# Kernel tuning notes

Measured on AMD Instinct MI355X. Metric: run time of the kernel, lower is better.

## Reference

```python
import jax, jax.numpy as jnp
import numpy as np
from jax import lax

SEQ_LEN, PRED_LEN, C_IN, D_MODEL, KS = 96, 48, 7, 128, 5
PAD = (KS - 1) // 2


def setup_inputs() -> dict:
    key = jax.random.key(0)
    ks = jax.random.split(key, 20)
    B = 512
    s = 0.02
    inp = {
        "x_enc": jax.random.normal(ks[0], (B, SEQ_LEN, C_IN), jnp.float32),
        "x_mark": jax.random.randint(ks[1], (B, SEQ_LEN, 4), 0, 7),
        "y_mark": jax.random.randint(ks[2], (B, SEQ_LEN + PRED_LEN, 4), 0, 7),
        # temporal embedding tables
        "hour_emb": jax.random.normal(ks[3], (24, D_MODEL)) * s,
        "weekday_emb": jax.random.normal(ks[4], (7, D_MODEL)) * s,
        "day_emb": jax.random.normal(ks[5], (32, D_MODEL)) * s,
        "month_emb": jax.random.normal(ks[6], (13, D_MODEL)) * s,
        # value embedding Linear(C_IN -> D_MODEL)
        "W_val": jax.random.normal(ks[7], (D_MODEL, C_IN)) * s,
        "b_val": jnp.zeros((D_MODEL,)),
        # three Conv1d(D_MODEL, D_MODEL, KS)
        "conv1_w": jax.random.normal(ks[8], (D_MODEL, D_MODEL, KS)) * s,
        "conv1_b": jnp.zeros((D_MODEL,)),
        "conv2_w": jax.random.normal(ks[9], (D_MODEL, D_MODEL, KS)) * s,
        "conv2_b": jnp.zeros((D_MODEL,)),
        "conv3_w": jax.random.normal(ks[10], (D_MODEL, D_MODEL, KS)) * s,
        "conv3_b": jnp.zeros((D_MODEL,)),
        # GRU (PyTorch layout: 3*D rows ordered [r, z, n])
        "gru_Wi": jax.random.normal(ks[11], (3 * D_MODEL, D_MODEL)) * s,
        "gru_Wh": jax.random.normal(ks[12], (3 * D_MODEL, D_MODEL)) * s,
        "gru_bi": jnp.zeros((3 * D_MODEL,)),
        "gru_bh": jnp.zeros((3 * D_MODEL,)),
        # fc Linear(D_MODEL -> C_IN)
        "fc_w": jax.random.normal(ks[13], (C_IN, D_MODEL)) * s,
        "fc_b": jnp.zeros((C_IN,)),
    }
    return inp


def _conv1d(x, w, b):
    # x: [B, D, T], w: [O, I, K]
    y = lax.conv_general_dilated(x, w, window_strides=(1,), padding=[(PAD, PAD)],
                                 dimension_numbers=("NCH", "OIH", "NCH"))
    return y + b[None, :, None]


def _gru_last(x, Wi, Wh, bi, bh):
    # x: [B, T, D] -> final hidden state [B, D] (PyTorch GRU equations)
    B, T, D = x.shape
    gx = jnp.einsum("btd,gd->btg", x, Wi) + bi  # [B, T, 3D]
    h0 = jnp.zeros((B, D), x.dtype)

    def step(h, gxt):
        gh = h @ Wh.T + bh
        r = jax.nn.sigmoid(gxt[:, :D] + gh[:, :D])
        z = jax.nn.sigmoid(gxt[:, D:2 * D] + gh[:, D:2 * D])
        n = jnp.tanh(gxt[:, 2 * D:] + r * gh[:, 2 * D:])
        return (1.0 - z) * n + z * h, None

    h_last, _ = lax.scan(step, h0, jnp.swapaxes(gx, 0, 1))
    return h_last


def reference(x_enc, x_mark, y_mark,
              hour_emb, weekday_emb, day_emb, month_emb,
              W_val, b_val,
              conv1_w, conv1_b, conv2_w, conv2_b, conv3_w, conv3_b,
              gru_Wi, gru_Wh, gru_bi, gru_bh, fc_w, fc_b):
    B = x_enc.shape[0]
    # temporal embedding for the full y_mark window (pointwise; precompute once)
    temb = (hour_emb[y_mark[:, :, 0]] + weekday_emb[y_mark[:, :, 1]]
            + day_emb[y_mark[:, :, 2]] + month_emb[y_mark[:, :, 3]])  # [B, L, D]

    x_cat = jnp.concatenate([x_enc, jnp.zeros((B, PRED_LEN, C_IN), x_enc.dtype)], axis=1)

    def one_step(x_cat, i):
        xw = lax.dynamic_slice(x_cat, (0, i, 0), (B, SEQ_LEN, C_IN))
        tw = lax.dynamic_slice(temb, (0, i, 0), (B, SEQ_LEN, D_MODEL))
        x = jnp.einsum("btc,dc->btd", xw, W_val) + b_val + tw  # [B, T, D]
        x = jnp.swapaxes(x, 1, 2)  # [B, D, T]
        x = jax.nn.relu(_conv1d(x, conv1_w, conv1_b))
        x = jax.nn.relu(_conv1d(x, conv2_w, conv2_b))
        x = jax.nn.relu(_conv1d(x, conv3_w, conv3_b))
        x = jnp.swapaxes(x, 1, 2)  # [B, T, D]
        h = _gru_last(x, gru_Wi, gru_Wh, gru_bi, gru_bh)  # [B, D]
        pred = h @ fc_w.T + fc_b  # [B, C]
        x_cat = lax.dynamic_update_slice(x_cat, pred[:, None, :], (0, SEQ_LEN + i, 0))
        return x_cat, None

    x_cat, _ = lax.scan(one_step, x_cat, jnp.arange(PRED_LEN))
    return x_cat[:, -PRED_LEN:, :]
```

## Files before the change

kernel.cpp:

```cpp
#include <hip/hip_runtime.h>

#define B_SZ 512
#define SEQ 96
#define PRED 48
#define TOT 144
#define CIN 7
#define DM 128
#define GDIM 384
#define KS 5

#define CSTR 132
#define ASUB (20*CSTR)
#define WROW 136
#define SWZ(o) ((o) + ((((o) >> 6)) << 2))

#define W_CONV (KS*DM*DM)
#define OFF_WIT (3*W_CONV)
#define OFF_WHT (3*W_CONV + DM*GDIM)
#define W_TOTAL (3*W_CONV + 2*DM*GDIM)

__device__ float g_gxg[(size_t)B_SZ*TOT*GDIM];
__device__ float g_gxe[B_SZ*12*GDIM];
__device__ float g_wT[W_TOTAL];

__global__ void prep_weights(const float* __restrict__ w1, const float* __restrict__ w2,
                             const float* __restrict__ w3, const float* __restrict__ Wi,
                             const float* __restrict__ Wh) {
    int tid = blockIdx.x*256 + threadIdx.x;
    if (tid < 3*W_CONV) {
        int l = tid / W_CONV, r = tid % W_CONV;
        int o = r & 127, c = (r >> 7) & 127, k = r >> 14;
        const float* w = (l==0) ? w1 : ((l==1) ? w2 : w3);
        g_wT[tid] = w[o*(DM*KS) + c*KS + k];
    } else if (tid < W_TOTAL) {
        int r = tid - 3*W_CONV;
        int m = r / (DM*GDIM), q = r % (DM*GDIM);
        int g = q % GDIM, c = q / GDIM;
        const float* W = (m==0) ? Wi : Wh;
        g_wT[tid] = W[g*DM + c];
    }
}

template<int NJ>
__device__ __forceinline__ void fma8(float (&acc)[NJ][8], int j, float a,
                                     const float4& wA, const float4& wB) {
    acc[j][0] = fmaf(a, wA.x, acc[j][0]);
    acc[j][1] = fmaf(a, wA.y, acc[j][1]);
    acc[j][2] = fmaf(a, wA.z, acc[j][2]);
    acc[j][3] = fmaf(a, wA.w, acc[j][3]);
    acc[j][4] = fmaf(a, wB.x, acc[j][4]);
    acc[j][5] = fmaf(a, wB.y, acc[j][5]);
    acc[j][6] = fmaf(a, wB.z, acc[j][6]);
    acc[j][7] = fmaf(a, wB.w, acc[j][7]);
}

__device__ __forceinline__ void stage_conv_chunk(float* __restrict__ wbuf,
                                                 const float* __restrict__ wT,
                                                 int cc, int tid) {
    const int cj = tid >> 5, oo = (tid & 31) * 4;
    #pragma unroll
    for (int k = 0; k < KS; ++k)
        *(float4*)(wbuf + (k*8 + cj)*WROW + SWZ(oo)) =
            *(const float4*)(wT + (k*DM + cc*8 + cj)*DM + oo);
}

__device__ __forceinline__ void stage_conv_chunk512(float* __restrict__ wbuf,
                                                    const float* __restrict__ wT,
                                                    int cc, int tid) {
    const int cj = tid >> 6, oo = (tid & 63) * 2;
    #pragma unroll
    for (int k = 0; k < KS; ++k)
        *(float2*)(wbuf + (k*8 + cj)*WROW + SWZ(oo)) =
            *(const float2*)(wT + (k*DM + cc*8 + cj)*DM + oo);
}

template<int NJ>
__device__ __forceinline__ void conv_layer_chunked(float* __restrict__ buf,
                                                   float* __restrict__ wbuf,
                                                   const float* __restrict__ wT,
                                                   const float* __restrict__ bias,
                                                   int nrow, int winO, int tid) {
    const int og = tid & 15, ttg = tid >> 4;
    const int o0 = og*8, so0 = SWZ(o0), r0 = ttg*NJ;
    const bool act = (r0 < nrow);
    float acc[NJ][8];
    #pragma unroll
    for (int u = 0; u < 8; ++u) {
        float bv = bias[o0+u];
        #pragma unroll
        for (int j = 0; j < NJ; ++j) acc[j][u] = bv;
    }
    for (int cc = 0; cc < DM/8; ++cc) {
        __syncthreads();
        stage_conv_chunk(wbuf, wT, cc, tid);
        __syncthreads();
        if (act) {
            const int c0 = cc*8;
            #pragma unroll
            for (int cj = 0; cj < 8; cj += 2) {
                float2 a2[NJ+4];
                #pragma unroll
                for (int m = 0; m < NJ+4; ++m)
                    a2[m] = *(const float2*)(buf + (r0+m)*CSTR + c0 + cj);
                #pragma unroll
                for (int k = 0; k < KS; ++k) {
                    const float4 wA0 = *(const float4*)(wbuf + (k*8+cj)*WROW + so0);
                    const float4 wB0 = *(const float4*)(wbuf + (k*8+cj)*WROW + so0 + 4);
                    const float4 wA1 = *(const float4*)(wbuf + (k*8+cj+1)*WROW + so0);
                    const float4 wB1 = *(const float4*)(wbuf + (k*8+cj+1)*WROW + so0 + 4);
                    #pragma unroll
                    for (int j = 0; j < NJ; ++j) {
                        fma8(acc, j, a2[j+k].x, wA0, wB0);
                        fma8(acc, j, a2[j+k].y, wA1, wB1);
                    }
                }
            }
        }
    }
    __syncthreads();
    if (act) {
        #pragma unroll
        for (int j = 0; j < NJ; ++j) {
            int q = r0 + j, w = winO + q;
            bool valid = (w >= 0) && (w < SEQ);
            #pragma unroll
            for (int u = 0; u < 8; ++u)
                buf[q*CSTR + o0+u] = valid ? fmaxf(acc[j][u], 0.f) : 0.f;
        }
    }
    __syncthreads();
}

__launch_bounds__(256, 3)
__global__ void init_kernel(const float* __restrict__ x_enc,
                            const int* __restrict__ y_mark,
                            const float* __restrict__ hour_e, const float* __restrict__ wk_e,
                            const float* __restrict__ day_e, const float* __restrict__ mon_e,
                            const float* __restrict__ W_val, const float* __restrict__ b_val,
                            const float* __restrict__ b1, const float* __restrict__ b2,
                            const float* __restrict__ b3, const float* __restrict__ gbi) {
    __shared__ float buf[60*CSTR];
    __shared__ float wbuf[KS*8*WROW];
    const int tid = threadIdx.x;
    const int b = blockIdx.x;
    const int cs = blockIdx.y * 48;

    for (int e = tid; e < 60*DM; e += 256) {
        int q = e >> 7, d = e & 127;
        int w = cs - 6 + q;
        float v = 0.f;
        if (w >= 0 && w < SEQ) {
            const float* xr = x_enc + (b*SEQ + w)*CIN;
            v = b_val[d];
            #pragma unroll
            for (int c = 0; c < CIN; ++c) v = fmaf(xr[c], W_val[d*CIN + c], v);
            const int* ym = y_mark + (b*TOT + w)*4;
            v += hour_e[ym[0]*DM + d] + wk_e[ym[1]*DM + d]
               + day_e[ym[2]*DM + d] + mon_e[ym[3]*DM + d];
        }
        buf[q*CSTR + d] = v;
    }
    conv_layer_chunked<4>(buf, wbuf, g_wT,            b1, 56, cs - 4, tid);
    conv_layer_chunked<4>(buf, wbuf, g_wT + W_CONV,   b2, 52, cs - 2, tid);
    conv_layer_chunked<3>(buf, wbuf, g_wT + 2*W_CONV, b3, 48, cs,     tid);

    const int og = tid & 15, ttg = tid >> 4;
    const int g0 = og*24, r0 = ttg*3;
    const float* WiT = g_wT + OFF_WIT;
    float ga[3][24];
    #pragma unroll
    for (int e = 0; e < 24; ++e) {
        float bv = gbi[g0+e];
        #pragma unroll
        for (int j = 0; j < 3; ++j) ga[j][e] = bv;
    }
    for (int cc = 0; cc < DM/8; ++cc) {
        __syncthreads();
        #pragma unroll
        for (int s = 0; s < 3; ++s)
            ((float4*)wbuf)[s*256 + tid] = ((const float4*)(WiT + cc*8*GDIM))[s*256 + tid];
        __syncthreads();
        const int c0 = cc*8;
        #pragma unroll
        for (int cj = 0; cj < 8; cj += 2) {
            float2 a2[3];
            #pragma unroll
            for (int m = 0; m < 3; ++m)
                a2[m] = *(const float2*)(buf + (r0+m)*CSTR + c0 + cj);
            float4 w4[6];
            #pragma unroll
            for (int q = 0; q < 6; ++q)
                w4[q] = *(const float4*)(wbuf + cj*GDIM + g0 + q*4);
            const float* wv = (const float*)w4;
            #pragma unroll
            for (int j = 0; j < 3; ++j)
                #pragma unroll
                for (int e = 0; e < 24; ++e)
                    ga[j][e] = fmaf(a2[j].x, wv[e], ga[j][e]);
            #pragma unroll
            for (int q = 0; q < 6; ++q)
                w4[q] = *(const float4*)(wbuf + (cj+1)*GDIM + g0 + q*4);
            #pragma unroll
            for (int j = 0; j < 3; ++j)
                #pragma unroll
                for (int e = 0; e < 24; ++e)
                    ga[j][e] = fmaf(a2[j].y, wv[e], ga[j][e]);
        }
    }
    #pragma unroll
    for (int j = 0; j < 3; ++j) {
        int w = cs + r0 + j;
        if (w >= 6 && w < 90) {
            float* gxo = g_gxg + ((size_t)b*TOT + w)*GDIM + g0;
            #pragma unroll
            for (int q = 0; q < 6; ++q)
                *(float4*)(gxo + q*4) = *(const float4*)&ga[j][q*4];
        }
    }
}

__device__ __forceinline__ void mlayer512(float* __restrict__ abuf, float* __restrict__ wbuf,
                                          const float* __restrict__ wT,
                                          const float* __restrict__ bias,
                                          int R, int off, int tid) {
    const int og = tid & 15, ttg = tid >> 4;
    const int o0 = og*8, so0 = SWZ(o0);
    const bool act = (ttg < 2*R);
    int s = 0, r0 = 0;
    if (act) { s = ttg / R; r0 = ttg - s*R; }
    float* in = abuf + s*ASUB;
    float acc[1][8];
    #pragma unroll
    for (int u = 0; u < 8; ++u) acc[0][u] = bias[o0+u];
    for (int cc = 0; cc < DM/8; ++cc) {
        __syncthreads();
        stage_conv_chunk512(wbuf, wT, cc, tid);
        __syncthreads();
        if (act) {
            const int c0 = cc*8;
            #pragma unroll
            for (int cj = 0; cj < 8; cj += 2) {
                float2 a2[5];
                #pragma unroll
                for (int m = 0; m < 5; ++m)
                    a2[m] = *(const float2*)(in + (r0+m)*CSTR + c0 + cj);
                #pragma unroll
                for (int k = 0; k < KS; ++k) {
                    const float4 wA0 = *(const float4*)(wbuf + (k*8+cj)*WROW + so0);
                    const float4 wB0 = *(const float4*)(wbuf + (k*8+cj)*WROW + so0 + 4);
                    const float4 wA1 = *(const float4*)(wbuf + (k*8+cj+1)*WROW + so0);
                    const float4 wB1 = *(const float4*)(wbuf + (k*8+cj+1)*WROW + so0 + 4);
                    fma8(acc, 0, a2[k].x, wA0, wB0);
                    fma8(acc, 0, a2[k].y, wA1, wB1);
                }
            }
        }
    }
    __syncthreads();
    if (act) {
        const int wb = s ? 83 : -6;
        int w = wb + off + r0;
        bool valid = (w >= 0) && (w < SEQ);
        #pragma unroll
        for (int u = 0; u < 8; ++u)
            in[r0*CSTR + o0+u] = valid ? fmaxf(acc[0][u], 0.f) : 0.f;
    }
    __syncthreads();
}

__launch_bounds__(512, 4)
__global__ void step512_kernel(int i, const float* __restrict__ x_enc,
                               const int* __restrict__ y_mark,
                               const float* __restrict__ hour_e, const float* __restrict__ wk_e,
                               const float* __restrict__ day_e, const float* __restrict__ mon_e,
                               const float* __restrict__ W_val, const float* __restrict__ b_val,
                               const float* __restrict__ b1, const float* __restrict__ b2,
                               const float* __restrict__ b3, const float* __restrict__ gbi,
                               const float* __restrict__ out) {
    __shared__ float abuf[2*ASUB];
    __shared__ float wbuf[16*GDIM];
    const int tid = threadIdx.x;
    const int b = blockIdx.x;

    for (int e = tid; e < 2*20*DM; e += 512) {
        int s = e / (20*DM);
        int rem = e - s*(20*DM);
        int q = rem >> 7, d = rem & 127;
        int w = (s ? 83 : -6) + q;
        float v = 0.f;
        if (w >= 0 && w < SEQ) {
            int p = i + w;
            const float* xr = (p < SEQ) ? (x_enc + (b*SEQ + p)*CIN)
                                        : (out + (b*PRED + (p - SEQ))*CIN);
            v = b_val[d];
            #pragma unroll
            for (int c = 0; c < CIN; ++c) v = fmaf(xr[c], W_val[d*CIN + c], v);
            const int* ym = y_mark + (b*TOT + p)*4;
            v += hour_e[ym[0]*DM + d] + wk_e[ym[1]*DM + d]
               + day_e[ym[2]*DM + d] + mon_e[ym[3]*DM + d];
        }
        abuf[s*ASUB + q*CSTR + d] = v;
    }
    mlayer512(abuf, wbuf, g_wT,            b1, 16, 2, tid);
    mlayer512(abuf, wbuf, g_wT + W_CONV,   b2, 12, 4, tid);
    mlayer512(abuf, wbuf, g_wT + 2*W_CONV, b3,  8, 6, tid);

    {
        const int row = tid >> 5;
        const int g0 = (tid & 31) * 12;
        const int ssub = row >> 3;
        const int r = row & 7;
        const float* a0p = abuf + ssub*ASUB + r*CSTR;
        const float* WiT = g_wT + OFF_WIT;
        float ga[12];
        #pragma unroll
        for (int e = 0; e < 12; ++e) ga[e] = gbi[g0+e];
        for (int cc = 0; cc < 8; ++cc) {
            __syncthreads();
            for (int x = tid; x < 16*GDIM/4; x += 512)
                ((float4*)wbuf)[x] = ((const float4*)(WiT + cc*16*GDIM))[x];
            __syncthreads();
            #pragma unroll
            for (int c = 0; c < 16; ++c) {
                float av = a0p[cc*16 + c];
                const float* wr = wbuf + c*GDIM + g0;
                #pragma unroll
                for (int q4 = 0; q4 < 3; ++q4) {
                    float4 w4 = *(const float4*)(wr + q4*4);
                    ga[q4*4+0] = fmaf(av, w4.x, ga[q4*4+0]);
                    ga[q4*4+1] = fmaf(av, w4.y, ga[q4*4+1]);
                    ga[q4*4+2] = fmaf(av, w4.z, ga[q4*4+2]);
                    ga[q4*4+3] = fmaf(av, w4.w, ga[q4*4+3]);
                }
            }
        }
        const int wb = ssub ? 83 : -6;
        int w = wb + 6 + r;
        float* dst = nullptr;
        if (ssub == 0) {
            if (w < 6) dst = g_gxe + ((size_t)b*12 + w)*GDIM + g0;
        } else {
            if (w == 89)      dst = g_gxg + ((size_t)b*TOT + (i + 89))*GDIM + g0;
            else if (w < SEQ) dst = g_gxe + ((size_t)b*12 + (w - 84))*GDIM + g0;
        }
        if (dst) {
            *(float4*)(dst)     = *(const float4*)&ga[0];
            *(float4*)(dst + 4) = *(const float4*)&ga[4];
            *(float4*)(dst + 8) = *(const float4*)&ga[8];
        }
    }
}

__launch_bounds__(512, 2)
__global__ void gru_rec(int i, const float* __restrict__ gbh,
                        const float* __restrict__ fc_w, const float* __restrict__ fc_b,
                        float* __restrict__ out) {
    __shared__ __align__(16) float H[2][DM];
    __shared__ float P[3][4][DM];
    const int tid = threadIdx.x;
    const int j = tid & 127, s = tid >> 7;
    const int b = blockIdx.x;

    float whr[32], whz[32], whn[32];
    {
        const float* Wp = g_wT + OFF_WHT + (size_t)(32*s)*GDIM + j;
        #pragma unroll
        for (int c = 0; c < 32; ++c) {
            whr[c] = Wp[c*GDIM];
            whz[c] = Wp[c*GDIM + DM];
            whn[c] = Wp[c*GDIM + 2*DM];
        }
    }

    const int cj = j;
    const bool comb = (tid < DM);
    float bhr = 0.f, bhz = 0.f, bhn = 0.f;
    if (comb) {
        bhr = gbh[cj]; bhz = gbh[DM + cj]; bhn = gbh[2*DM + cj];
        H[0][cj] = 0.f;
    }

    const float* gxg_b = g_gxg + (size_t)b*TOT*GDIM;
    const float* gxe_b = g_gxe + (size_t)b*12*GDIM;
    auto gp = [&](int t) -> const float* {
        return (t < 6)  ? (gxe_b + t*GDIM)
             : (t < 90) ? (gxg_b + (size_t)(i + t)*GDIM)
                        : (gxe_b + (t - 84)*GDIM);
    };

    float gxr = 0.f, gxz = 0.f, gxn = 0.f;
    if (comb) {
        const float* g0p = gp(0);
        gxr = g0p[cj]; gxz = g0p[DM + cj]; gxn = g0p[2*DM + cj];
    }
    __syncthreads();

    for (int t = 0; t < SEQ; ++t) {
        {
            const float* Hc = &H[t & 1][32*s];
            float ar = 0.f, az = 0.f, an = 0.f;
            #pragma unroll
            for (int c = 0; c < 32; c += 4) {
                float4 h4 = *(const float4*)(Hc + c);
                ar = fmaf(h4.x, whr[c],   ar); az = fmaf(h4.x, whz[c],   az); an = fmaf(h4.x, whn[c],   an);
                ar = fmaf(h4.y, whr[c+1], ar); az = fmaf(h4.y, whz[c+1], az); an = fmaf(h4.y, whn[c+1], an);
                ar = fmaf(h4.z, whr[c+2], ar); az = fmaf(h4.z, whz[c+2], az); an = fmaf(h4.z, whn[c+2], an);
                ar = fmaf(h4.w, whr[c+3], ar); az = fmaf(h4.w, whz[c+3], az); an = fmaf(h4.w, whn[c+3], an);
            }
            P[0][s][j] = ar;
            P[1][s][j] = az;
            P[2][s][j] = an;
        }
        __syncthreads();
        if (comb) {
            float ar = bhr + ((P[0][0][cj] + P[0][1][cj]) + (P[0][2][cj] + P[0][3][cj]));
            float az = bhz + ((P[1][0][cj] + P[1][1][cj]) + (P[1][2][cj] + P[1][3][cj]));
            float an = bhn + ((P[2][0][cj] + P[2][1][cj]) + (P[2][2][cj] + P[2][3][cj]));
            float r = 1.f/(1.f + __expf(-(gxr + ar)));
            float z = 1.f/(1.f + __expf(-(gxz + az)));
            float xn = gxn + r*an;
            float e2 = __expf(2.f*xn);
            float n = 1.f - 2.f/(e2 + 1.f);
            float h = (1.f - z)*n + z*H[t & 1][cj];
            H[(t + 1) & 1][cj] = h;
            if (t + 1 < SEQ) {
                const float* gq = gp(t + 1);
                gxr = gq[cj]; gxz = gq[DM + cj]; gxn = gq[2*DM + cj];
            }
        }
        __syncthreads();
    }

    if (tid < CIN) {
        int o = tid;
        float p = fc_b[o];
        const float* Hf = H[0];
        #pragma unroll
        for (int d = 0; d < DM; ++d) p = fmaf(fc_w[o*DM + d], Hf[d], p);
        out[(b*PRED + i)*CIN + o] = p;
    }
}

extern "C" void kernel_launch(void* const* d_in, const int* in_sizes, int n_in,
                              void* d_out, int out_size, void* d_ws, size_t ws_size,
                              hipStream_t stream) {
    const float* x_enc  = (const float*)d_in[0];
    const int*   y_mark = (const int*)d_in[2];
    const float* hour_e = (const float*)d_in[3];
    const float* wk_e   = (const float*)d_in[4];
    const float* day_e  = (const float*)d_in[5];
    const float* mon_e  = (const float*)d_in[6];
    const float* W_val  = (const float*)d_in[7];
    const float* b_val  = (const float*)d_in[8];
    const float* c1w    = (const float*)d_in[9];
    const float* c1b    = (const float*)d_in[10];
    const float* c2w    = (const float*)d_in[11];
    const float* c2b    = (const float*)d_in[12];
    const float* c3w    = (const float*)d_in[13];
    const float* c3b    = (const float*)d_in[14];
    const float* Wi     = (const float*)d_in[15];
    const float* Wh     = (const float*)d_in[16];
    const float* gbi    = (const float*)d_in[17];
    const float* gbh    = (const float*)d_in[18];
    const float* fcw    = (const float*)d_in[19];
    const float* fcb    = (const float*)d_in[20];
    float* out = (float*)d_out;

    prep_weights<<<(W_TOTAL + 255)/256, 256, 0, stream>>>(c1w, c2w, c3w, Wi, Wh);

    init_kernel<<<dim3(B_SZ, 2), 256, 0, stream>>>(x_enc, y_mark,
        hour_e, wk_e, day_e, mon_e, W_val, b_val, c1b, c2b, c3b, gbi);

    for (int i = 0; i < PRED; ++i) {
        step512_kernel<<<B_SZ, 512, 0, stream>>>(i, x_enc, y_mark,
            hour_e, wk_e, day_e, mon_e, W_val, b_val, c1b, c2b, c3b, gbi, out);
        gru_rec<<<B_SZ, 512, 0, stream>>>(i, gbh, fcw, fcb, out);
    }
}
```

Measured before the change: 12.30 ms.

## Fuse per-step conv/input-projection kernel with GRU recurrence kernel

```diff
diff --git a/kernel.cpp b/kernel.cpp
--- a/kernel.cpp
+++ b/kernel.cpp
@@ -20,7 +20,6 @@
 #define W_TOTAL (3*W_CONV + 2*DM*GDIM)
 
 __device__ float g_gxg[(size_t)B_SZ*TOT*GDIM];
-__device__ float g_gxe[B_SZ*12*GDIM];
 __device__ float g_wT[W_TOTAL];
 
 __global__ void prep_weights(const float* __restrict__ w1, const float* __restrict__ w2,
@@ -268,15 +267,17 @@
     __syncthreads();
 }
 
-__launch_bounds__(512, 4)
-__global__ void step512_kernel(int i, const float* __restrict__ x_enc,
-                               const int* __restrict__ y_mark,
-                               const float* __restrict__ hour_e, const float* __restrict__ wk_e,
-                               const float* __restrict__ day_e, const float* __restrict__ mon_e,
-                               const float* __restrict__ W_val, const float* __restrict__ b_val,
-                               const float* __restrict__ b1, const float* __restrict__ b2,
-                               const float* __restrict__ b3, const float* __restrict__ gbi,
-                               const float* __restrict__ out) {
+__launch_bounds__(512, 2)
+__global__ void fstep_kernel(int i, const float* __restrict__ x_enc,
+                             const int* __restrict__ y_mark,
+                             const float* __restrict__ hour_e, const float* __restrict__ wk_e,
+                             const float* __restrict__ day_e, const float* __restrict__ mon_e,
+                             const float* __restrict__ W_val, const float* __restrict__ b_val,
+                             const float* __restrict__ b1, const float* __restrict__ b2,
+                             const float* __restrict__ b3, const float* __restrict__ gbi,
+                             const float* __restrict__ gbh,
+                             const float* __restrict__ fc_w, const float* __restrict__ fc_b,
+                             float* __restrict__ out) {
     __shared__ float abuf[2*ASUB];
     __shared__ float wbuf[16*GDIM];
     const int tid = threadIdx.x;
@@ -305,6 +306,7 @@
     mlayer512(abuf, wbuf, g_wT + W_CONV,   b2, 12, 4, tid);
     mlayer512(abuf, wbuf, g_wT + 2*W_CONV, b3,  8, 6, tid);
 
+    float* const gxe = abuf;
     {
         const int row = tid >> 5;
         const int g0 = (tid & 31) * 12;
@@ -334,33 +336,34 @@
                 }
             }
         }
+        __syncthreads();
         const int wb = ssub ? 83 : -6;
         int w = wb + 6 + r;
-        float* dst = nullptr;
+        float* dst0 = nullptr;
+        float* dst1 = nullptr;
         if (ssub == 0) {
-            if (w < 6) dst = g_gxe + ((size_t)b*12 + w)*GDIM + g0;
+            if (w < 6) dst0 = gxe + w*GDIM + g0;
         } else {
-            if (w == 89)      dst = g_gxg + ((size_t)b*TOT + (i + 89))*GDIM + g0;
-            else if (w < SEQ) dst = g_gxe + ((size_t)b*12 + (w - 84))*GDIM + g0;
-        }
-        if (dst) {
-            *(float4*)(dst)     = *(const float4*)&ga[0];
-            *(float4*)(dst + 4) = *(const float4*)&ga[4];
-            *(float4*)(dst + 8) = *(const float4*)&ga[8];
-        }
-    }
-}
-
-__launch_bounds__(512, 2)
-__global__ void gru_rec(int i, const float* __restrict__ gbh,
-                        const float* __restrict__ fc_w, const float* __restrict__ fc_b,
-                        float* __restrict__ out) {
-    __shared__ __align__(16) float H[2][DM];
-    __shared__ float P[3][4][DM];
-    const int tid = threadIdx.x;
+            if (w == 89) {
+                dst0 = gxe + 6*GDIM + g0;
+                dst1 = g_gxg + ((size_t)b*TOT + (i + 89))*GDIM + g0;
+            } else if (w < SEQ) {
+                dst0 = gxe + (6 + w - 89)*GDIM + g0;
+            }
+        }
+        if (dst0) {
+            *(float4*)(dst0)     = *(const float4*)&ga[0];
+            *(float4*)(dst0 + 4) = *(const float4*)&ga[4];
+            *(float4*)(dst0 + 8) = *(const float4*)&ga[8];
+        }
+        if (dst1) {
+            *(float4*)(dst1)     = *(const float4*)&ga[0];
+            *(float4*)(dst1 + 4) = *(const float4*)&ga[4];
+            *(float4*)(dst1 + 8) = *(const float4*)&ga[8];
+        }
+    }
+
     const int j = tid & 127, s = tid >> 7;
-    const int b = blockIdx.x;
-
     float whr[32], whz[32], whn[32];
     {
         const float* Wp = g_wT + OFF_WHT + (size_t)(32*s)*GDIM + j;
@@ -370,34 +373,35 @@
             whz[c] = Wp[c*GDIM + DM];
             whn[c] = Wp[c*GDIM + 2*DM];
         }
-    }
-
+        #pragma unroll
+        for (int c = 0; c < 32; ++c)
+            asm volatile("" : "+v"(whr[c]), "+v"(whz[c]), "+v"(whn[c]));
+    }
+    float* const Hb = wbuf;
+    float* const Pb = wbuf + 2*DM;
     const int cj = j;
     const bool comb = (tid < DM);
     float bhr = 0.f, bhz = 0.f, bhn = 0.f;
-    if (comb) {
-        bhr = gbh[cj]; bhz = gbh[DM + cj]; bhn = gbh[2*DM + cj];
-        H[0][cj] = 0.f;
-    }
+    if (comb) { bhr = gbh[cj]; bhz = gbh[DM + cj]; bhn = gbh[2*DM + cj]; }
+    if (tid < 2*DM) Hb[tid] = 0.f;
 
     const float* gxg_b = g_gxg + (size_t)b*TOT*GDIM;
-    const float* gxe_b = g_gxe + (size_t)b*12*GDIM;
     auto gp = [&](int t) -> const float* {
-        return (t < 6)  ? (gxe_b + t*GDIM)
-             : (t < 90) ? (gxg_b + (size_t)(i + t)*GDIM)
-                        : (gxe_b + (t - 84)*GDIM);
+        return (t < 6)  ? (gxe + t*GDIM)
+             : (t < 89) ? (gxg_b + (size_t)(i + t)*GDIM)
+                        : (gxe + (6 + t - 89)*GDIM);
     };
 
+    __syncthreads();
     float gxr = 0.f, gxz = 0.f, gxn = 0.f;
     if (comb) {
         const float* g0p = gp(0);
         gxr = g0p[cj]; gxz = g0p[DM + cj]; gxn = g0p[2*DM + cj];
     }
-    __syncthreads();
 
     for (int t = 0; t < SEQ; ++t) {
         {
-            const float* Hc = &H[t & 1][32*s];
+            const float* Hc = Hb + (t & 1)*DM + 32*s;
             float ar = 0.f, az = 0.f, an = 0.f;
             #pragma unroll
             for (int c = 0; c < 32; c += 4) {
@@ -407,22 +411,22 @@
                 ar = fmaf(h4.z, whr[c+2], ar); az = fmaf(h4.z, whz[c+2], az); an = fmaf(h4.z, whn[c+2], an);
                 ar = fmaf(h4.w, whr[c+3], ar); az = fmaf(h4.w, whz[c+3], az); an = fmaf(h4.w, whn[c+3], an);
             }
-            P[0][s][j] = ar;
-            P[1][s][j] = az;
-            P[2][s][j] = an;
+            Pb[(0*4 + s)*DM + j] = ar;
+            Pb[(1*4 + s)*DM + j] = az;
+            Pb[(2*4 + s)*DM + j] = an;
         }
         __syncthreads();
         if (comb) {
-            float ar = bhr + ((P[0][0][cj] + P[0][1][cj]) + (P[0][2][cj] + P[0][3][cj]));
-            float az = bhz + ((P[1][0][cj] + P[1][1][cj]) + (P[1][2][cj] + P[1][3][cj]));
-            float an = bhn + ((P[2][0][cj] + P[2][1][cj]) + (P[2][2][cj] + P[2][3][cj]));
+            float ar = bhr + ((Pb[(0*4+0)*DM+cj] + Pb[(0*4+1)*DM+cj]) + (Pb[(0*4+2)*DM+cj] + Pb[(0*4+3)*DM+cj]));
+            float az = bhz + ((Pb[(1*4+0)*DM+cj] + Pb[(1*4+1)*DM+cj]) + (Pb[(1*4+2)*DM+cj] + Pb[(1*4+3)*DM+cj]));
+            float an = bhn + ((Pb[(2*4+0)*DM+cj] + Pb[(2*4+1)*DM+cj]) + (Pb[(2*4+2)*DM+cj] + Pb[(2*4+3)*DM+cj]));
             float r = 1.f/(1.f + __expf(-(gxr + ar)));
             float z = 1.f/(1.f + __expf(-(gxz + az)));
             float xn = gxn + r*an;
             float e2 = __expf(2.f*xn);
             float n = 1.f - 2.f/(e2 + 1.f);
-            float h = (1.f - z)*n + z*H[t & 1][cj];
-            H[(t + 1) & 1][cj] = h;
+            float h = (1.f - z)*n + z*Hb[(t & 1)*DM + cj];
+            Hb[((t + 1) & 1)*DM + cj] = h;
             if (t + 1 < SEQ) {
                 const float* gq = gp(t + 1);
                 gxr = gq[cj]; gxz = gq[DM + cj]; gxn = gq[2*DM + cj];
@@ -434,9 +438,8 @@
     if (tid < CIN) {
         int o = tid;
         float p = fc_b[o];
-        const float* Hf = H[0];
-        #pragma unroll
-        for (int d = 0; d < DM; ++d) p = fmaf(fc_w[o*DM + d], Hf[d], p);
+        #pragma unroll
+        for (int d = 0; d < DM; ++d) p = fmaf(fc_w[o*DM + d], Hb[d], p);
         out[(b*PRED + i)*CIN + o] = p;
     }
 }
@@ -472,8 +475,8 @@
         hour_e, wk_e, day_e, mon_e, W_val, b_val, c1b, c2b, c3b, gbi);
 
     for (int i = 0; i < PRED; ++i) {
-        step512_kernel<<<B_SZ, 512, 0, stream>>>(i, x_enc, y_mark,
-            hour_e, wk_e, day_e, mon_e, W_val, b_val, c1b, c2b, c3b, gbi, out);
-        gru_rec<<<B_SZ, 512, 0, stream>>>(i, gbh, fcw, fcb, out);
-    }
-}
+        fstep_kernel<<<B_SZ, 512, 0, stream>>>(i, x_enc, y_mark,
+            hour_e, wk_e, day_e, mon_e, W_val, b_val, c1b, c2b, c3b,
+            gbi, gbh, fcw, fcb, out);
+    }
+}
```

Result: slower. 17.41 ms (+41.5%).
